# Optimization experiments

Hardware: AMD Instinct MI355X
Metric: run time of the kernel (lower is better)

The kernel has to match this reference:

```python
import jax, jax.numpy as jnp
import numpy as np

DIM = 192; NH = 6; WS = 8; SS = 4
D_INNER = 384; D_STATE = 64; MNH = 6; HEADDIM = 64; DCONV = 4; CHUNK = 128


def layernorm(x, w, b):
    m = jnp.mean(x, axis=-1, keepdims=True)
    v = jnp.var(x, axis=-1, keepdims=True)
    return (x - m) * jax.lax.rsqrt(v + 1e-5) * w + b


def segsum(a):
    # a: (..., T) -> (..., T, T) with [i,j] = sum_{k=j+1..i} a_k (lower-tri), -inf-ish above diag
    T = a.shape[-1]
    x = jnp.broadcast_to(a[..., None], a.shape + (T,))
    lo = np.tril(np.ones((T, T), dtype=bool), -1)
    x = jnp.where(lo, x, 0.0)
    s = jnp.cumsum(x, axis=-2)
    keep = np.tril(np.ones((T, T), dtype=bool), 0)
    return jnp.where(keep, s, -1e9)


def ssd(X, a, Bm, Cm):
    # Mamba2 chunked state-space dual scan. X:(b,l,h,p) a:(b,l,h) Bm/Cm:(b,l,n)
    b, l, h, p = X.shape
    n = Bm.shape[-1]
    nc = l // CHUNK
    Xc = X.reshape(b, nc, CHUNK, h, p)
    ac = a.reshape(b, nc, CHUNK, h).transpose(0, 3, 1, 2)  # (b,h,c,cl)
    Bc = Bm.reshape(b, nc, CHUNK, n)
    Cc = Cm.reshape(b, nc, CHUNK, n)
    a_cs = jnp.cumsum(ac, axis=-1)
    Lm = jnp.exp(segsum(ac))  # (b,h,c,cl,cl)
    Y_diag = jnp.einsum('bcln,bcsn,bhcls,bcshp->bclhp', Cc, Bc, Lm, Xc)
    decay_states = jnp.exp(a_cs[..., -1:] - a_cs)
    states = jnp.einsum('bcln,bhcl,bclhp->bchpn', Bc, decay_states, Xc)
    a_last = jnp.pad(a_cs[..., -1], ((0, 0), (0, 0), (1, 0)))
    decay_chunk = jnp.exp(segsum(a_last))  # (b,h,c+1,c+1)
    states_cat = jnp.concatenate([jnp.zeros_like(states[:, :1]), states], axis=1)
    prev = jnp.einsum('bhzc,bchpn->bzhpn', decay_chunk, states_cat)[:, :-1]
    Y_off = jnp.einsum('bcln,bchpn,bhcl->bclhp', Cc, prev, jnp.exp(a_cs))
    return (Y_diag + Y_off).reshape(b, l, h, p)


def mamba2(xs, in_w, conv_w, conv_b, dt_bias, A_log, D, norm_w, out_w):
    b, l, _ = xs.shape
    zxbcdt = xs @ in_w.T  # (b,l,2*di+2*n+nh)
    z = zxbcdt[..., :D_INNER]
    xBC = zxbcdt[..., D_INNER:2 * D_INNER + 2 * D_STATE]
    dt = jax.nn.softplus(zxbcdt[..., -MNH:] + dt_bias)
    # causal depthwise conv1d
    xt = xBC.transpose(0, 2, 1)
    xt = jax.lax.conv_general_dilated(xt, conv_w[:, None, :], (1,), [(DCONV - 1, 0)],
                                      feature_group_count=xt.shape[1],
                                      dimension_numbers=('NCH', 'OIH', 'NCH'))
    xBC = jax.nn.silu((xt + conv_b[None, :, None]).transpose(0, 2, 1))
    xp = xBC[..., :D_INNER].reshape(b, l, MNH, HEADDIM)
    Bm = xBC[..., D_INNER:D_INNER + D_STATE]
    Cm = xBC[..., D_INNER + D_STATE:]
    A = -jnp.exp(A_log)
    y = ssd(xp * dt[..., None], dt * A, Bm, Cm)
    y = y + xp * D[None, None, :, None]
    y = y.reshape(b, l, D_INNER)
    y = y * jax.nn.silu(z)  # gated RMSNorm
    y = y * jax.lax.rsqrt(jnp.mean(y * y, axis=-1, keepdims=True) + 1e-5) * norm_w
    return y @ out_w.T


def build_mask(H, W):
    img = np.zeros((H, W))
    cnt = 0
    for hs in (slice(0, -WS), slice(-WS, -SS), slice(-SS, None)):
        for wsl in (slice(0, -WS), slice(-WS, -SS), slice(-SS, None)):
            img[hs, wsl] = cnt
            cnt += 1
    mw = img.reshape(H // WS, WS, W // WS, WS).transpose(0, 2, 1, 3).reshape(-1, WS * WS)
    diff = mw[:, None, :] - mw[:, :, None]
    return jnp.asarray(np.where(diff != 0, -100.0, 0.0).astype(np.float32))


def gated_window_attn(xw, mask, qkv_w, qkv_b, proj_w, proj_b, gate_w, gate_b):
    Bw, N, C = xw.shape
    hd = C // NH
    qkv = (xw @ qkv_w.T + qkv_b).reshape(Bw, N, 3, NH, hd).transpose(2, 0, 3, 1, 4)
    q, k, v = qkv[0], qkv[1], qkv[2]
    s = jnp.einsum('bhnd,bhmd->bhnm', q, k) * (hd ** -0.5)
    nW = mask.shape[0]
    s = (s.reshape(Bw // nW, nW, NH, N, N) + mask[None, :, None]).reshape(Bw, NH, N, N)
    a = jax.nn.softmax(s, axis=-1)
    o = jnp.einsum('bhnm,bhmd->bhnd', a, v).transpose(0, 2, 1, 3)  # (Bw,N,NH,hd)
    gate = jax.nn.sigmoid(xw @ gate_w.T + gate_b)  # per-head gate from pre-attn x
    o = (o * gate[..., None]).reshape(Bw, N, C)
    return o @ proj_w.T + proj_b


def lgs_forward(x, H, W, n1_w, n1_b, m_in_w, m_conv_w, m_conv_b, m_dt_bias, m_A_log,
                m_D, m_norm_w, m_out_w, qkv_w, qkv_b, proj_w, proj_b, gate_w, gate_b,
                fus_w, fus_b, eca_w, n2_w, n2_b, fc1_w, fc1_b, fc2_w, fc2_b):
    twoB, L, C = x.shape
    Bh = twoB // 2
    shortcut = x
    xn = layernorm(x, n1_w, n1_b)
    # Mamba branch: interleave frame0/frame1 tokens -> (Bh, 2L, C) scan -> de-interleave
    xs = jnp.stack([xn[:Bh], xn[Bh:]], axis=2).reshape(Bh, 2 * L, C)
    ym = mamba2(xs, m_in_w, m_conv_w, m_conv_b, m_dt_bias, m_A_log, m_D, m_norm_w, m_out_w)
    ym = ym.reshape(Bh, L, 2, C)
    x_mamba = jnp.concatenate([ym[:, :, 0], ym[:, :, 1]], axis=0)  # (2B,L,C)
    # shifted-window gated attention branch
    x2 = jnp.roll(xn.reshape(twoB, H, W, C), (-SS, -SS), axis=(1, 2))
    xw = x2.reshape(twoB, H // WS, WS, W // WS, WS, C).transpose(0, 1, 3, 2, 4, 5).reshape(-1, WS * WS, C)
    ow = gated_window_attn(xw, build_mask(H, W), qkv_w, qkv_b, proj_w, proj_b, gate_w, gate_b)
    ow = ow.reshape(twoB, H // WS, W // WS, WS, WS, C).transpose(0, 1, 3, 2, 4, 5).reshape(twoB, H, W, C)
    x_attn = jnp.roll(ow, (SS, SS), axis=(1, 2)).reshape(twoB, L, C)
    # fusion 1x1 conv == per-pixel linear over concatenated channels
    xf = jnp.concatenate([x_mamba, x_attn], axis=-1) @ fus_w.T + fus_b
    # ECAB: global-avg-pool channel attention via k=3 1D conv over channels
    pooled = jnp.pad(jnp.mean(xf, axis=1), ((0, 0), (1, 1)))
    ca = jax.nn.sigmoid(eca_w[0] * pooled[:, :-2] + eca_w[1] * pooled[:, 1:-1] + eca_w[2] * pooled[:, 2:])
    xf = xf * ca[:, None, :]
    xo = shortcut + xf
    h = layernorm(xo, n2_w, n2_b)
    h = jax.nn.gelu(h @ fc1_w.T + fc1_b, approximate=False) @ fc2_w.T + fc2_b
    return xo + h


def setup_inputs() -> dict:
    key = jax.random.key(0)
    ks = jax.random.split(key, 12)
    C = DIM

    def w(k, shape, s=0.02):
        return jax.random.normal(k, shape, jnp.float32) * s

    return {
        'x': jax.random.normal(ks[0], (4, 2304, C), jnp.float32),
        'H': 48, 'W': 48,
        'n1_w': jnp.ones((C,), jnp.float32), 'n1_b': jnp.zeros((C,), jnp.float32),
        'm_in_w': w(ks[1], (2 * D_INNER + 2 * D_STATE + MNH, C)),
        'm_conv_w': w(ks[2], (D_INNER + 2 * D_STATE, DCONV), 0.1),
        'm_conv_b': jnp.zeros((D_INNER + 2 * D_STATE,), jnp.float32),
        'm_dt_bias': jnp.log(jnp.expm1(jnp.full((MNH,), 0.01, jnp.float32))),
        'm_A_log': jnp.log(jnp.arange(1, MNH + 1, dtype=jnp.float32)),
        'm_D': jnp.ones((MNH,), jnp.float32),
        'm_norm_w': jnp.ones((D_INNER,), jnp.float32),
        'm_out_w': w(ks[3], (C, D_INNER)),
        'qkv_w': w(ks[4], (3 * C, C)), 'qkv_b': jnp.zeros((3 * C,), jnp.float32),
        'proj_w': w(ks[5], (C, C)), 'proj_b': jnp.zeros((C,), jnp.float32),
        'gate_w': w(ks[6], (NH, C)), 'gate_b': jnp.zeros((NH,), jnp.float32),
        'fus_w': w(ks[7], (C, 2 * C)), 'fus_b': jnp.zeros((C,), jnp.float32),
        'eca_w': w(ks[8], (3,), 0.3),
        'n2_w': jnp.ones((C,), jnp.float32), 'n2_b': jnp.zeros((C,), jnp.float32),
        'fc1_w': w(ks[9], (4 * C, C)), 'fc1_b': jnp.zeros((4 * C,), jnp.float32),
        'fc2_w': w(ks[10], (C, 4 * C)), 'fc2_b': jnp.zeros((C,), jnp.float32),
    }


def reference(x, H, W, n1_w, n1_b, m_in_w, m_conv_w, m_conv_b, m_dt_bias, m_A_log,
              m_D, m_norm_w, m_out_w, qkv_w, qkv_b, proj_w, proj_b, gate_w, gate_b,
              fus_w, fus_b, eca_w, n2_w, n2_b, fc1_w, fc1_b, fc2_w, fc2_b):
    return lgs_forward(x, H, W, n1_w, n1_b, m_in_w, m_conv_w, m_conv_b, m_dt_bias,
                       m_A_log, m_D, m_norm_w, m_out_w, qkv_w, qkv_b, proj_w, proj_b,
                       gate_w, gate_b, fus_w, fus_b, eca_w, n2_w, n2_b,
                       fc1_w, fc1_b, fc2_w, fc2_b)
```

## Files before the change

kernel.cpp:

```cpp
#include <hip/hip_runtime.h>
#include <math.h>

#define DEV __device__ __forceinline__

typedef __attribute__((ext_vector_type(8))) short short8;
typedef __attribute__((ext_vector_type(4))) float f32x4;

DEV float sigmoidf_(float x){ return 1.f/(1.f+__expf(-x)); }
DEV float siluf_(float x){ return x/(1.f+__expf(-x)); }
DEV float softplusf_(float x){ return (x>20.f)? x : log1pf(__expf(x)); }

DEV short bf16rne(float f){
  unsigned u=__float_as_uint(f);
  unsigned r=(u + 0x7FFFu + ((u>>16)&1u))>>16;
  return (short)r;
}
DEV unsigned short bf16u(float f){ return (unsigned short)bf16rne(f); }
DEV float b2f(unsigned short u){ return __uint_as_float(((unsigned)u)<<16); }
DEV float b2fs(short u){ return __uint_as_float(((unsigned)(unsigned short)u)<<16); }

DEV void gll16(const void* g, void* l){
  __builtin_amdgcn_global_load_lds(
      (const __attribute__((address_space(1))) void*)g,
      (__attribute__((address_space(3))) void*)(unsigned)(uintptr_t)l,
      16, 0, 0);
}

DEV int map_row(int r, int mode){
  if(mode==1){
    int b=r/4608; int gl=r-b*4608;
    return ((gl&1)*2+b)*2304 + (gl>>1);
  }
  if(mode==2){
    int widx=r>>6, n=r&63;
    int b=widx/36, t=widx-b*36;
    int wi=t/6, wj=t-wi*6;
    int h2=wi*8+(n>>3), w2=wj*8+(n&7);
    int ho=h2+4; if(ho>=48) ho-=48;
    int wo=w2+4; if(wo>=48) wo-=48;
    return b*2304 + ho*48 + wo;
  }
  return r;
}

__global__ __launch_bounds__(256) void k_w2b(const float* __restrict__ w0,const float* __restrict__ w1,
    const float* __restrict__ w2,const float* __restrict__ w3,const float* __restrict__ w4,
    const float* __restrict__ w5,const float* __restrict__ w6, short* __restrict__ dst){
  int seg=blockIdx.y;
  int i=blockIdx.x*256+threadIdx.x;
  const float* src; int size, off;
  switch(seg){
    case 0: src=w0; size=173184; off=0;      break;
    case 1: src=w1; size=110592; off=173184; break;
    case 2: src=w2; size=73728;  off=283776; break;
    case 3: src=w3; size=36864;  off=357504; break;
    case 4: src=w4; size=73728;  off=394368; break;
    case 5: src=w5; size=147456; off=468096; break;
    default:src=w6; size=147456; off=615552; break;
  }
  if(i<size) dst[off+i]=bf16rne(src[i]);
}

__global__ __launch_bounds__(256) void k_ln(const float* __restrict__ in, const float* __restrict__ w,
                                            const float* __restrict__ b, short* __restrict__ out){
  int warp=threadIdx.x>>6, lane=threadIdx.x&63;
  int row=blockIdx.x*4+warp;
  const float* ip=in+(size_t)row*192;
  float v0=ip[lane], v1=ip[lane+64], v2=ip[lane+128];
  float s=v0+v1+v2, sq=v0*v0+v1*v1+v2*v2;
  #pragma unroll
  for(int off=32;off;off>>=1){ s+=__shfl_xor(s,off); sq+=__shfl_xor(sq,off); }
  float mean=s*(1.f/192.f), var=sq*(1.f/192.f)-mean*mean;
  float inv=rsqrtf(var+1e-5f);
  short* op=out+(size_t)row*192;
  op[lane]    =bf16rne((v0-mean)*inv*w[lane]    +b[lane]);
  op[lane+64] =bf16rne((v1-mean)*inv*w[lane+64] +b[lane+64]);
  op[lane+128]=bf16rne((v2-mean)*inv*w[lane+128]+b[lane+128]);
}

template<int K>
__global__ __launch_bounds__(256,4) void k_gemm(const short* __restrict__ A, const short* __restrict__ W,
    const float* __restrict__ bias, const float* __restrict__ res,
    float* __restrict__ Of, short* __restrict__ Ob,
    int N, int ldo, int col_off, int gmode, int smode, int epi){
  constexpr int NP=K/64;
  __shared__ short sMem[16384];
  short (*sA)[64][64]=(short(*)[64][64])sMem;
  short (*sB)[64][64]=(short(*)[64][64])(sMem+8192);
  float* sO=(float*)sMem;
  int tid=threadIdx.x, lane=tid&63, wid=tid>>6;
  int m16=lane&15, kq=lane>>4;
  int bm=blockIdx.x*64, bn=blockIdx.y*64;
  int lrow=lane>>3;
  int lcol=((lane&7)^lrow)<<3;
  int sx=(m16&7)<<3;
  const short* ap[2]; const short* wp[2];
  #pragma unroll
  for(int t=0;t<2;t++){
    int i8=wid+t*4;
    int arow=map_row(bm+i8*8+lrow,gmode);
    ap[t]=A+(size_t)arow*K+lcol;
    int n=bn+i8*8+lrow;
    if(n>=N) n=N-1;
    wp[t]=W+(size_t)n*K+lcol;
  }
  f32x4 acc[4];
  #pragma unroll
  for(int ni=0;ni<4;ni++) acc[ni]=(f32x4){0.f,0.f,0.f,0.f};

  auto stage=[&](int p,int b){
    #pragma unroll
    for(int t=0;t<2;t++){
      int i8=wid+t*4;
      gll16(ap[t]+p*64, &sA[b][i8*8][0]);
      gll16(wp[t]+p*64, &sB[b][i8*8][0]);
    }
  };
  auto compute=[&](int p,int b){
    __builtin_amdgcn_s_setprio(1);
    #pragma unroll
    for(int half=0;half<2;half++){
      int k2=(half*32 + kq*8) ^ sx;
      short8 af=*(const short8*)&sA[b][wid*16+m16][k2];
      #pragma unroll
      for(int ni=0;ni<4;ni++){
        short8 bf=*(const short8*)&sB[b][ni*16+m16][k2];
        acc[ni]=__builtin_amdgcn_mfma_f32_16x16x32_bf16(af,bf,acc[ni],0,0,0);
      }
    }
    __builtin_amdgcn_s_setprio(0);
  };

  stage(0,0);
  if(NP>1) stage(1,1);
  #pragma unroll
  for(int p=0;p<NP;p++){
    if(p+1<NP) asm volatile("s_waitcnt vmcnt(4)":::"memory");
    else       asm volatile("s_waitcnt vmcnt(0)":::"memory");
    __builtin_amdgcn_s_barrier();
    compute(p,p&1);
    if(p+2<NP){
      __builtin_amdgcn_s_barrier();
      stage(p+2,p&1);
    }
  }

  __syncthreads();
  {
    int mbase=wid*16+4*kq;
    #pragma unroll
    for(int ni=0;ni<4;ni++)
      #pragma unroll
      for(int r=0;r<4;r++)
        sO[(mbase+r)*65 + ni*16+m16]=acc[ni][r];
  }
  __syncthreads();
  int erow=tid>>3, c0=(tid&7)*8;
  #pragma unroll
  for(int rd=0;rd<2;rd++){
    int ml=rd*32+erow;
    int m=bm+ml;
    int orow=map_row(m,smode);
    float v[8];
    #pragma unroll
    for(int j=0;j<8;j++) v[j]=sO[ml*65+c0+j];
    const float* rp=res? res+(size_t)orow*ldo+col_off : nullptr;
    #pragma unroll
    for(int j=0;j<8;j++){
      int nn=bn+c0+j;
      float val=v[j];
      if(bias && nn<N) val+=bias[nn];
      if(epi==2) val=0.5f*val*(1.f+erff(val*0.70710678118654752f));
      else if(epi==3) val+=rp[nn];
      v[j]=val;
    }
    size_t obase=(size_t)orow*ldo+col_off+bn+c0;
    if(bn+c0+7<N){
      if(Ob){
        short8 w;
        #pragma unroll
        for(int j=0;j<8;j++) w[j]=bf16rne(v[j]);
        *(short8*)(Ob+obase)=w;
      } else {
        float4 f0={v[0],v[1],v[2],v[3]}, f1={v[4],v[5],v[6],v[7]};
        *(float4*)(Of+obase)=f0;
        *(float4*)(Of+obase+4)=f1;
      }
    } else {
      #pragma unroll
      for(int j=0;j<8;j++){
        int nn=bn+c0+j;
        if(nn<N){ if(Ob) Ob[obase+j]=bf16rne(v[j]); else Of[obase+j]=v[j]; }
      }
    }
  }
}

__global__ __launch_bounds__(256) void k_conv(const short* __restrict__ zx, const float* __restrict__ cw,
                       const float* __restrict__ cb, short* __restrict__ xbc){
  int idx=blockIdx.x*256+threadIdx.x;
  if(idx>=2*4608*64) return;
  int ch0=(idx&63)*8; int rl=idx>>6;
  int l=rl%4608;
  const short* base=zx+(size_t)rl*904+384+ch0;
  short8 x0=*(const short8*)(base);
  short8 x1={0,0,0,0,0,0,0,0},x2=x1,x3=x1;
  if(l>=1) x1=*(const short8*)(base-904);
  if(l>=2) x2=*(const short8*)(base-2*904);
  if(l>=3) x3=*(const short8*)(base-3*904);
  short8 out;
  #pragma unroll
  for(int j=0;j<8;j++){
    float4 w=*(const float4*)(cw+(ch0+j)*4);
    float acc=cb[ch0+j]
      + b2fs(x3[j])*w.x + b2fs(x2[j])*w.y + b2fs(x1[j])*w.z + b2fs(x0[j])*w.w;
    out[j]=bf16rne(siluf_(acc));
  }
  *(short8*)(xbc+(size_t)rl*512+ch0)=out;
}

__global__ __launch_bounds__(128) void k_prep(const short* __restrict__ zx, const float* __restrict__ dt_bias,
    const float* __restrict__ A_log, float* __restrict__ dtb, float* __restrict__ acs, float* __restrict__ csum){
  int bid=blockIdx.x;
  int c=bid%36, h=(bid/36)%6, b=bid/216;
  int l=threadIdx.x;
  int row=b*4608+c*128+l;
  float xv=b2fs(zx[(size_t)row*904+896+h])+dt_bias[h];
  float dt=softplusf_(xv);
  float a=-__expf(A_log[h])*dt;
  dtb[row*6+h]=dt;
  __shared__ float sb[128];
  sb[l]=a; __syncthreads();
  for(int off=1;off<128;off<<=1){
    float add=(l>=off)? sb[l-off]:0.f;
    __syncthreads();
    sb[l]+=add;
    __syncthreads();
  }
  acs[((size_t)(b*6+h)*36+c)*128+l]=sb[l];
  if(l==127) csum[(b*6+h)*36+c]=sb[127];
}

__global__ __launch_bounds__(256) void k_ssd_a(const short* __restrict__ xbc, const float* __restrict__ dtb,
    const float* __restrict__ acs, const float* __restrict__ csum,
    short* __restrict__ st, float* __restrict__ Y){
  int bid=blockIdx.x;
  int h=bid%6, c=(bid/6)%36, b=bid/216;
  __shared__ unsigned short sB[128][68];
  __shared__ unsigned short sC[128][68];
  __shared__ unsigned short sXdT[64][132];
  __shared__ unsigned short sBTE[64][132];
  __shared__ unsigned short sM[128][36];
  __shared__ float sAcs[128];
  __shared__ float sE[128];
  int tid=threadIdx.x;
  int lane=tid&63, wid=tid>>6;
  int m16=lane&15, kq=lane>>4;
  int base_row=b*4608+c*128;
  const float* acsp=acs+((size_t)(b*6+h)*36+c)*128;
  float tot=csum[(b*6+h)*36+c];
  if(tid<128){ float a=acsp[tid]; sAcs[tid]=a; sE[tid]=__expf(tot-a); }
  __syncthreads();
  for(int i=tid;i<1024;i+=256){
    int l=i>>3, n0=(i&7)*8;
    int row=base_row+l;
    const short* rp=xbc+(size_t)row*512;
    short8 Bv=*(const short8*)(rp+384+n0);
    short8 Cv=*(const short8*)(rp+448+n0);
    short8 Xv=*(const short8*)(rp+h*64+n0);
    float dt=dtb[row*6+h];
    float e=sE[l];
    *(short8*)&sB[l][n0]=Bv;
    *(short8*)&sC[l][n0]=Cv;
    #pragma unroll
    for(int j=0;j<8;j++){
      sXdT[n0+j][l]=bf16u(b2fs(Xv[j])*dt);
      sBTE[n0+j][l]=bf16u(b2fs(Bv[j])*e);
    }
  }
  __syncthreads();
  {
    int wr=wid>>1, wc=wid&1;
    f32x4 accS[2][2];
    #pragma unroll
    for(int mi=0;mi<2;mi++)
      #pragma unroll
      for(int ni=0;ni<2;ni++) accS[mi][ni]=(f32x4){0.f,0.f,0.f,0.f};
    #pragma unroll
    for(int ks=0;ks<4;ks++){
      short8 a0=*(const short8*)&sXdT[wr*32+m16][ks*32+kq*8];
      short8 a1=*(const short8*)&sXdT[wr*32+16+m16][ks*32+kq*8];
      short8 b0=*(const short8*)&sBTE[wc*32+m16][ks*32+kq*8];
      short8 b1=*(const short8*)&sBTE[wc*32+16+m16][ks*32+kq*8];
      accS[0][0]=__builtin_amdgcn_mfma_f32_16x16x32_bf16(a0,b0,accS[0][0],0,0,0);
      accS[0][1]=__builtin_amdgcn_mfma_f32_16x16x32_bf16(a0,b1,accS[0][1],0,0,0);
      accS[1][0]=__builtin_amdgcn_mfma_f32_16x16x32_bf16(a1,b0,accS[1][0],0,0,0);
      accS[1][1]=__builtin_amdgcn_mfma_f32_16x16x32_bf16(a1,b1,accS[1][1],0,0,0);
    }
    short* op=st+((size_t)((b*36+c)*6+h))*4096;
    #pragma unroll
    for(int mi=0;mi<2;mi++)
      #pragma unroll
      for(int ni=0;ni<2;ni++)
        #pragma unroll
        for(int r=0;r<4;r++){
          int p=wr*32+mi*16+4*kq+r, n=wc*32+ni*16+m16;
          op[p*64+n]=bf16rne(accS[mi][ni][r]);
        }
  }
  #pragma unroll
  for(int ti=0;ti<2;ti++){
    int t = ti? (7-wid) : wid;
    f32x4 accY[4];
    #pragma unroll
    for(int pi=0;pi<4;pi++) accY[pi]=(f32x4){0.f,0.f,0.f,0.f};
    int nslab=(t>>1)+1;
    for(int jt=0;jt<nslab;jt++){
      f32x4 accD[2];
      accD[0]=(f32x4){0.f,0.f,0.f,0.f}; accD[1]=(f32x4){0.f,0.f,0.f,0.f};
      #pragma unroll
      for(int ks=0;ks<2;ks++){
        short8 a =*(const short8*)&sC[t*16+m16][ks*32+kq*8];
        short8 b0=*(const short8*)&sB[jt*32+m16][ks*32+kq*8];
        short8 b1=*(const short8*)&sB[jt*32+16+m16][ks*32+kq*8];
        accD[0]=__builtin_amdgcn_mfma_f32_16x16x32_bf16(a,b0,accD[0],0,0,0);
        accD[1]=__builtin_amdgcn_mfma_f32_16x16x32_bf16(a,b1,accD[1],0,0,0);
      }
      int lrow=t*16+4*kq;
      #pragma unroll
      for(int sti=0;sti<2;sti++)
        #pragma unroll
        for(int r=0;r<4;r++){
          int l=lrow+r, s=jt*32+sti*16+m16;
          float v=(s<=l)? __expf(sAcs[l]-sAcs[s])*accD[sti][r] : 0.f;
          sM[l][sti*16+m16]=bf16u(v);
        }
      short8 am=*(const short8*)&sM[t*16+m16][kq*8];
      #pragma unroll
      for(int pi=0;pi<4;pi++){
        short8 bx=*(const short8*)&sXdT[pi*16+m16][jt*32+kq*8];
        accY[pi]=__builtin_amdgcn_mfma_f32_16x16x32_bf16(am,bx,accY[pi],0,0,0);
      }
    }
    #pragma unroll
    for(int pi=0;pi<4;pi++)
      #pragma unroll
      for(int r=0;r<4;r++){
        int l=t*16+4*kq+r, p=pi*16+m16;
        Y[(size_t)(base_row+l)*384+h*64+p]=accY[pi][r];
      }
  }
}

__global__ __launch_bounds__(256) void k_scan(const short* __restrict__ st, const float* __restrict__ csum,
                                              short* __restrict__ prevb){
  int bid=blockIdx.x;
  int seg=bid&15, bh=bid>>4;
  int b=bh/6, h=bh%6;
  __shared__ float sE[36];
  if(threadIdx.x<36) sE[threadIdx.x]=__expf(csum[(b*6+h)*36+threadIdx.x]);
  __syncthreads();
  int e=seg*256+threadIdx.x;
  size_t stride=(size_t)6*4096;
  size_t idx=((size_t)((b*36+0)*6+h))*4096+e;
  float carry=0.f;
  for(int c4=0;c4<36;c4+=4){
    float v[4];
    #pragma unroll
    for(int j=0;j<4;j++) v[j]=b2fs(st[idx+j*stride]);
    #pragma unroll
    for(int j=0;j<4;j++){
      prevb[idx+j*stride]=bf16rne(carry);
      carry=carry*sE[c4+j]+v[j];
    }
    idx+=4*stride;
  }
}

__global__ __launch_bounds__(256) void k_ssd_b(const short* __restrict__ xbc, const short* __restrict__ prevb,
    const float* __restrict__ acs, const float* __restrict__ Dv, float* __restrict__ Y){
  int bid=blockIdx.x;
  int h=bid%6, c=(bid/6)%36, b=bid/216;
  __shared__ unsigned short sC[128][68];
  __shared__ unsigned short sP[64][68];
  __shared__ float sAcs[128];
  int tid=threadIdx.x;
  int lane=tid&63, wid=tid>>6;
  int m16=lane&15, kq=lane>>4;
  int base_row=b*4608+c*128;
  const float* acsp=acs+((size_t)(b*6+h)*36+c)*128;
  if(tid<128) sAcs[tid]=acsp[tid];
  for(int i=tid;i<1024;i+=256){
    int l=i>>3, n0=(i&7)*8;
    short8 Cv=*(const short8*)(xbc+(size_t)(base_row+l)*512+448+n0);
    *(short8*)&sC[l][n0]=Cv;
  }
  const short* pp=prevb+((size_t)((b*36+c)*6+h))*4096;
  for(int i=tid;i<512;i+=256){
    int p_=i>>3, n0=(i&7)*8;
    short8 Pv=*(const short8*)(pp+p_*64+n0);
    *(short8*)&sP[p_][n0]=Pv;
  }
  __syncthreads();
  float Dh=Dv[h];
  int lt0=2*wid;
  f32x4 acc[2][4];
  #pragma unroll
  for(int li=0;li<2;li++)
    #pragma unroll
    for(int pi=0;pi<4;pi++) acc[li][pi]=(f32x4){0.f,0.f,0.f,0.f};
  #pragma unroll
  for(int ks=0;ks<2;ks++){
    short8 a0=*(const short8*)&sC[lt0*16+m16][ks*32+kq*8];
    short8 a1=*(const short8*)&sC[(lt0+1)*16+m16][ks*32+kq*8];
    #pragma unroll
    for(int pi=0;pi<4;pi++){
      short8 bp=*(const short8*)&sP[pi*16+m16][ks*32+kq*8];
      acc[0][pi]=__builtin_amdgcn_mfma_f32_16x16x32_bf16(a0,bp,acc[0][pi],0,0,0);
      acc[1][pi]=__builtin_amdgcn_mfma_f32_16x16x32_bf16(a1,bp,acc[1][pi],0,0,0);
    }
  }
  #pragma unroll
  for(int li=0;li<2;li++){
    #pragma unroll
    for(int r=0;r<4;r++){
      int l=(lt0+li)*16+4*kq+r;
      int row=base_row+l;
      float e=__expf(sAcs[l]);
      #pragma unroll
      for(int pi=0;pi<4;pi++){
        int p=pi*16+m16;
        size_t yi=(size_t)row*384+h*64+p;
        float xpv=b2fs(xbc[(size_t)row*512+h*64+p]);
        Y[yi]+=acc[li][pi][r]*e+xpv*Dh;
      }
    }
  }
}

__global__ __launch_bounds__(256) void k_rmsgate(const float* __restrict__ Y, const short* __restrict__ zx,
    const float* __restrict__ nw, short* __restrict__ yn){
  int warp=threadIdx.x>>6, lane=threadIdx.x&63;
  int row=blockIdx.x*4+warp;
  float v[6]; float ss=0.f;
  #pragma unroll
  for(int j=0;j<6;j++){
    int cidx=lane+64*j;
    float y=Y[(size_t)row*384+cidx];
    float z=b2fs(zx[(size_t)row*904+cidx]);
    y*=siluf_(z);
    v[j]=y; ss+=y*y;
  }
  #pragma unroll
  for(int off=32;off;off>>=1) ss+=__shfl_xor(ss,off);
  float sc=rsqrtf(ss*(1.f/384.f)+1e-5f);
  #pragma unroll
  for(int j=0;j<6;j++){
    int cidx=lane+64*j;
    yn[(size_t)row*384+cidx]=bf16rne(v[j]*sc*nw[cidx]);
  }
}

__global__ __launch_bounds__(128) void k_att2(const short* __restrict__ qkv, const short* __restrict__ xn,
    const float* __restrict__ gw, const float* __restrict__ gb, short* __restrict__ obuf){
  int bid=blockIdx.x;
  int widx=bid/6, head=bid-widx*6;
  int b=widx/36, t=widx-b*36;
  int wi=t/6, wj=t-wi*6;
  int n=threadIdx.x&63, half=threadIdx.x>>6;
  __shared__ float sK[64][32], sV[64][32];
  __shared__ float sO2[64][32];
  __shared__ float sM2[64], sD2[64];
  const short* qp=qkv+(size_t)(widx*64+n)*576+head*32;
  float q[32];
  {
    short8 v0=*(const short8*)(qp),    v1=*(const short8*)(qp+8);
    short8 v2=*(const short8*)(qp+16), v3=*(const short8*)(qp+24);
    #pragma unroll
    for(int i=0;i<8;i++){ q[i]=b2fs(v0[i]); q[8+i]=b2fs(v1[i]); q[16+i]=b2fs(v2[i]); q[24+i]=b2fs(v3[i]); }
    short8 k0=*(const short8*)(qp+192+half*16), k1=*(const short8*)(qp+200+half*16);
    short8 u0=*(const short8*)(qp+384+half*16), u1=*(const short8*)(qp+392+half*16);
    #pragma unroll
    for(int i=0;i<8;i++){
      sK[n][half*16+i]=b2fs(k0[i]); sK[n][half*16+8+i]=b2fs(k1[i]);
      sV[n][half*16+i]=b2fs(u0[i]); sV[n][half*16+8+i]=b2fs(u1[i]);
    }
  }
  int h2=wi*8+(n>>3), w2=wj*8+(n&7);
  int rh=(h2<40)?0:((h2<44)?1:2);
  int rw=(w2<40)?0:((w2<44)?1:2);
  int myid=rh*3+rw;
  __syncthreads();
  const float scale=0.17677669529663687f;
  float p[32]; float mx=-1e30f;
  #pragma unroll 4
  for(int jj=0;jj<32;jj++){
    int j=half*32+jj;
    float sc=0;
    #pragma unroll
    for(int d=0;d<32;d++) sc+=q[d]*sK[j][d];
    int hj=wi*8+(j>>3), wjj=wj*8+(j&7);
    int rhj=(hj<40)?0:((hj<44)?1:2);
    int rwj=(wjj<40)?0:((wjj<44)?1:2);
    float m=((rhj*3+rwj)!=myid)? -100.f:0.f;
    float v=sc*scale+m;
    p[jj]=v; mx=fmaxf(mx,v);
  }
  float den=0;
  #pragma unroll
  for(int jj=0;jj<32;jj++){ p[jj]=__expf(p[jj]-mx); den+=p[jj]; }
  float o[32];
  #pragma unroll
  for(int d=0;d<32;d++) o[d]=0.f;
  #pragma unroll 4
  for(int jj=0;jj<32;jj++){
    float pj=p[jj];
    #pragma unroll
    for(int d=0;d<32;d++) o[d]+=pj*sV[half*32+jj][d];
  }
  if(half==1){
    sM2[n]=mx; sD2[n]=den;
    #pragma unroll
    for(int d=0;d<32;d++) sO2[n][d]=o[d];
  }
  __syncthreads();
  if(half==0){
    float m1=sM2[n], d1=sD2[n];
    float m=fmaxf(mx,m1);
    float e0=__expf(mx-m), e1=__expf(m1-m);
    float dent=den*e0+d1*e1;
    int xrow=map_row(widx*64+n,2);
    const short* xp=xn+(size_t)xrow*192;
    const float* gwp=gw+head*192;
    float g=0;
    #pragma unroll
    for(int c=0;c<24;c++){
      short8 xv=*(const short8*)(xp+c*8);
      float4 w0=*(const float4*)(gwp+c*8);
      float4 w1=*(const float4*)(gwp+c*8+4);
      g+=b2fs(xv[0])*w0.x+b2fs(xv[1])*w0.y+b2fs(xv[2])*w0.z+b2fs(xv[3])*w0.w
        +b2fs(xv[4])*w1.x+b2fs(xv[5])*w1.y+b2fs(xv[6])*w1.z+b2fs(xv[7])*w1.w;
    }
    g=sigmoidf_(g+gb[head]);
    float fac=g/dent;
    short* op=obuf+(size_t)(widx*64+n)*192+head*32;
    #pragma unroll
    for(int v8=0;v8<4;v8++){
      short8 w;
      #pragma unroll
      for(int j=0;j<8;j++){
        int d=v8*8+j;
        w[j]=bf16rne((o[d]*e0+sO2[n][d]*e1)*fac);
      }
      *(short8*)(op+v8*8)=w;
    }
  }
}

__global__ __launch_bounds__(192) void k_pool1(const float* __restrict__ xf, float* __restrict__ partial){
  int bid=blockIdx.x; int b=bid/18, seg=bid%18;
  int cidx=threadIdx.x;
  const float* p=xf+((size_t)b*2304+seg*128)*192+cidx;
  float s=0;
  for(int l=0;l<128;l++) s+=p[(size_t)l*192];
  partial[bid*192+cidx]=s;
}

__global__ __launch_bounds__(768) void k_ca(const float* __restrict__ partial, const float* __restrict__ ecaw,
                                            float* __restrict__ ca){
  int tid=threadIdx.x;
  int b=tid/192, cidx=tid%192;
  float s=0;
  for(int k=0;k<18;k++) s+=partial[(b*18+k)*192+cidx];
  float pv=s*(1.f/2304.f);
  __shared__ float sP[768];
  sP[tid]=pv; __syncthreads();
  float left =(cidx>0)?   sP[tid-1]:0.f;
  float right=(cidx<191)? sP[tid+1]:0.f;
  ca[tid]=sigmoidf_(ecaw[0]*left+ecaw[1]*pv+ecaw[2]*right);
}

__global__ __launch_bounds__(256) void k_xoln(const float* __restrict__ x, const float* __restrict__ xf,
    const float* __restrict__ ca, const float* __restrict__ w, const float* __restrict__ bvec,
    float* __restrict__ xo, short* __restrict__ out){
  int warp=threadIdx.x>>6, lane=threadIdx.x&63;
  int row=blockIdx.x*4+warp;
  int bidx=row/2304;
  const float* cap=ca+bidx*192;
  const float* xp=x+(size_t)row*192;
  const float* fp=xf+(size_t)row*192;
  float v0=xp[lane]    +fp[lane]    *cap[lane];
  float v1=xp[lane+64] +fp[lane+64] *cap[lane+64];
  float v2=xp[lane+128]+fp[lane+128]*cap[lane+128];
  float* op=xo+(size_t)row*192;
  op[lane]=v0; op[lane+64]=v1; op[lane+128]=v2;
  float s=v0+v1+v2, sq=v0*v0+v1*v1+v2*v2;
  #pragma unroll
  for(int off=32;off;off>>=1){ s+=__shfl_xor(s,off); sq+=__shfl_xor(sq,off); }
  float mean=s*(1.f/192.f), var=sq*(1.f/192.f)-mean*mean;
  float inv=rsqrtf(var+1e-5f);
  short* bp=out+(size_t)row*192;
  bp[lane]    =bf16rne((v0-mean)*inv*w[lane]    +bvec[lane]);
  bp[lane+64] =bf16rne((v1-mean)*inv*w[lane+64] +bvec[lane+64]);
  bp[lane+128]=bf16rne((v2-mean)*inv*w[lane+128]+bvec[lane+128]);
}

extern "C" void kernel_launch(void* const* d_in, const int* in_sizes, int n_in,
                              void* d_out, int out_size, void* d_ws, size_t ws_size,
                              hipStream_t stream){
  const float* x     =(const float*)d_in[0];
  const float* n1w   =(const float*)d_in[3];
  const float* n1b   =(const float*)d_in[4];
  const float* m_in_w=(const float*)d_in[5];
  const float* m_cw  =(const float*)d_in[6];
  const float* m_cb  =(const float*)d_in[7];
  const float* m_dtb =(const float*)d_in[8];
  const float* m_Al  =(const float*)d_in[9];
  const float* m_D   =(const float*)d_in[10];
  const float* m_nw  =(const float*)d_in[11];
  const float* m_ow  =(const float*)d_in[12];
  const float* qkvw  =(const float*)d_in[13];
  const float* qkvb  =(const float*)d_in[14];
  const float* projw =(const float*)d_in[15];
  const float* projb =(const float*)d_in[16];
  const float* gatew =(const float*)d_in[17];
  const float* gateb =(const float*)d_in[18];
  const float* fusw  =(const float*)d_in[19];
  const float* fusb  =(const float*)d_in[20];
  const float* ecaw  =(const float*)d_in[21];
  const float* n2w   =(const float*)d_in[22];
  const float* n2b   =(const float*)d_in[23];
  const float* fc1w  =(const float*)d_in[24];
  const float* fc1b  =(const float*)d_in[25];
  const float* fc2w  =(const float*)d_in[26];
  const float* fc2b  =(const float*)d_in[27];
  float* out=(float*)d_out;
  float* ws=(float*)d_ws;

  short* xn_bf  = (short*)(ws + 0);
  short* wb     = (short*)(ws + 884736);
  short* zx_bf  = (short*)(ws + 1266240);
  short* xbc_bf = (short*)(ws + 5431872);
  float* dtb    = ws + 7791168;
  float* acs    = ws + 7846464;
  float* csum   = ws + 7901760;
  short* st_bf  = (short*)(ws + 7902272);
  short* prevb_bf=(short*)(ws + 9671744);
  float* Y      = ws + 11441216;
  float* bigbf  = ws + 14980160;
  short* hbuf_bf= xn_bf;
  short* obuf_bf= xbc_bf;
  short* xcat_bf= prevb_bf;
  float* xf     = (float*)st_bf;
  float* xo     = Y;
  short* yn_bf  = (short*)bigbf;
  short* qkv_bf = (short*)bigbf;
  short* h1_bf  = (short*)bigbf;
  float* partial= dtb;
  float* ca     = acs;
  short* wb_in  = wb + 0;
  short* wb_qkv = wb + 173184;
  short* wb_out = wb + 283776;
  short* wb_proj= wb + 357504;
  short* wb_fus = wb + 394368;
  short* wb_fc1 = wb + 468096;
  short* wb_fc2 = wb + 615552;

  k_w2b<<<dim3(677,7),256,0,stream>>>(m_in_w,qkvw,m_ow,projw,fusw,fc1w,fc2w,wb);
  k_ln<<<2304,256,0,stream>>>(x,n1w,n1b,xn_bf);
  k_gemm<192><<<dim3(144,15),256,0,stream>>>(xn_bf,wb_in,nullptr,nullptr,nullptr,zx_bf, 902,904,0, 1,0,0);
  k_conv<<<2304,256,0,stream>>>(zx_bf,m_cw,m_cb,xbc_bf);
  k_prep<<<432,128,0,stream>>>(zx_bf,m_dtb,m_Al,dtb,acs,csum);
  k_ssd_a<<<432,256,0,stream>>>(xbc_bf,dtb,acs,csum,st_bf,Y);
  k_scan<<<192,256,0,stream>>>(st_bf,csum,prevb_bf);
  k_ssd_b<<<432,256,0,stream>>>(xbc_bf,prevb_bf,acs,m_D,Y);
  k_rmsgate<<<2304,256,0,stream>>>(Y,zx_bf,m_nw,yn_bf);
  k_gemm<384><<<dim3(144,3),256,0,stream>>>(yn_bf,wb_out,nullptr,nullptr,nullptr,xcat_bf, 192,384,0, 0,1,0);
  k_gemm<192><<<dim3(144,9),256,0,stream>>>(xn_bf,wb_qkv,qkvb,nullptr,nullptr,qkv_bf, 576,576,0, 2,0,0);
  k_att2<<<864,128,0,stream>>>(qkv_bf,xn_bf,gatew,gateb,obuf_bf);
  k_gemm<192><<<dim3(144,3),256,0,stream>>>(obuf_bf,wb_proj,projb,nullptr,nullptr,xcat_bf, 192,384,192, 0,2,0);
  k_gemm<384><<<dim3(144,3),256,0,stream>>>(xcat_bf,wb_fus,fusb,nullptr,xf,nullptr, 192,192,0, 0,0,0);
  k_pool1<<<72,192,0,stream>>>(xf,partial);
  k_ca<<<1,768,0,stream>>>(partial,ecaw,ca);
  k_xoln<<<2304,256,0,stream>>>(x,xf,ca,n2w,n2b,xo,hbuf_bf);
  k_gemm<192><<<dim3(144,12),256,0,stream>>>(hbuf_bf,wb_fc1,fc1b,nullptr,nullptr,h1_bf, 768,768,0, 0,0,2);
  k_gemm<768><<<dim3(144,3),256,0,stream>>>(h1_bf,wb_fc2,fc2b,xo,out,nullptr, 192,192,0, 0,0,3);
}
```

Baseline: 175.1 us.

## Fuse small kernels, store Y in bf16, fold pooling into fusion GEMM

```diff
diff --git a/kernel.cpp b/kernel.cpp
--- a/kernel.cpp
+++ b/kernel.cpp
@@ -43,46 +43,12 @@
   return r;
 }
 
-__global__ __launch_bounds__(256) void k_w2b(const float* __restrict__ w0,const float* __restrict__ w1,
-    const float* __restrict__ w2,const float* __restrict__ w3,const float* __restrict__ w4,
-    const float* __restrict__ w5,const float* __restrict__ w6, short* __restrict__ dst){
-  int seg=blockIdx.y;
-  int i=blockIdx.x*256+threadIdx.x;
-  const float* src; int size, off;
-  switch(seg){
-    case 0: src=w0; size=173184; off=0;      break;
-    case 1: src=w1; size=110592; off=173184; break;
-    case 2: src=w2; size=73728;  off=283776; break;
-    case 3: src=w3; size=36864;  off=357504; break;
-    case 4: src=w4; size=73728;  off=394368; break;
-    case 5: src=w5; size=147456; off=468096; break;
-    default:src=w6; size=147456; off=615552; break;
-  }
-  if(i<size) dst[off+i]=bf16rne(src[i]);
-}
-
-__global__ __launch_bounds__(256) void k_ln(const float* __restrict__ in, const float* __restrict__ w,
-                                            const float* __restrict__ b, short* __restrict__ out){
-  int warp=threadIdx.x>>6, lane=threadIdx.x&63;
-  int row=blockIdx.x*4+warp;
-  const float* ip=in+(size_t)row*192;
-  float v0=ip[lane], v1=ip[lane+64], v2=ip[lane+128];
-  float s=v0+v1+v2, sq=v0*v0+v1*v1+v2*v2;
-  #pragma unroll
-  for(int off=32;off;off>>=1){ s+=__shfl_xor(s,off); sq+=__shfl_xor(sq,off); }
-  float mean=s*(1.f/192.f), var=sq*(1.f/192.f)-mean*mean;
-  float inv=rsqrtf(var+1e-5f);
-  short* op=out+(size_t)row*192;
-  op[lane]    =bf16rne((v0-mean)*inv*w[lane]    +b[lane]);
-  op[lane+64] =bf16rne((v1-mean)*inv*w[lane+64] +b[lane+64]);
-  op[lane+128]=bf16rne((v2-mean)*inv*w[lane+128]+b[lane+128]);
-}
-
 template<int K>
-__global__ __launch_bounds__(256,4) void k_gemm(const short* __restrict__ A, const short* __restrict__ W,
+DEV void gemm_body(const short* __restrict__ A, const short* __restrict__ W,
     const float* __restrict__ bias, const float* __restrict__ res,
     float* __restrict__ Of, short* __restrict__ Ob,
-    int N, int ldo, int col_off, int gmode, int smode, int epi){
+    int N, int ldo, int col_off, int gmode, int smode, int epi,
+    int bx, int by, float* __restrict__ pool){
   constexpr int NP=K/64;
   __shared__ short sMem[16384];
   short (*sA)[64][64]=(short(*)[64][64])sMem;
@@ -90,7 +56,7 @@
   float* sO=(float*)sMem;
   int tid=threadIdx.x, lane=tid&63, wid=tid>>6;
   int m16=lane&15, kq=lane>>4;
-  int bm=blockIdx.x*64, bn=blockIdx.y*64;
+  int bm=bx*64, bn=by*64;
   int lrow=lane>>3;
   int lcol=((lane&7)^lrow)<<3;
   int sx=(m16&7)<<3;
@@ -194,56 +160,127 @@
       }
     }
   }
-}
-
-__global__ __launch_bounds__(256) void k_conv(const short* __restrict__ zx, const float* __restrict__ cw,
-                       const float* __restrict__ cb, short* __restrict__ xbc){
-  int idx=blockIdx.x*256+threadIdx.x;
-  if(idx>=2*4608*64) return;
-  int ch0=(idx&63)*8; int rl=idx>>6;
-  int l=rl%4608;
-  const short* base=zx+(size_t)rl*904+384+ch0;
-  short8 x0=*(const short8*)(base);
-  short8 x1={0,0,0,0,0,0,0,0},x2=x1,x3=x1;
-  if(l>=1) x1=*(const short8*)(base-904);
-  if(l>=2) x2=*(const short8*)(base-2*904);
-  if(l>=3) x3=*(const short8*)(base-3*904);
-  short8 out;
-  #pragma unroll
-  for(int j=0;j<8;j++){
-    float4 w=*(const float4*)(cw+(ch0+j)*4);
-    float acc=cb[ch0+j]
-      + b2fs(x3[j])*w.x + b2fs(x2[j])*w.y + b2fs(x1[j])*w.z + b2fs(x0[j])*w.w;
-    out[j]=bf16rne(siluf_(acc));
-  }
-  *(short8*)(xbc+(size_t)rl*512+ch0)=out;
-}
-
-__global__ __launch_bounds__(128) void k_prep(const short* __restrict__ zx, const float* __restrict__ dt_bias,
-    const float* __restrict__ A_log, float* __restrict__ dtb, float* __restrict__ acs, float* __restrict__ csum){
+  if(pool){
+    if(tid<64){
+      float s=0;
+      #pragma unroll 8
+      for(int ml=0;ml<64;ml++) s+=sO[ml*65+tid];
+      if(bias) s+=64.f*bias[bn+tid];
+      atomicAdd(&pool[(bm/2304)*192 + bn+tid], s);
+    }
+  }
+}
+
+template<int K>
+__global__ __launch_bounds__(256,4) void k_gemm(const short* __restrict__ A, const short* __restrict__ W,
+    const float* __restrict__ bias, const float* __restrict__ res,
+    float* __restrict__ Of, short* __restrict__ Ob,
+    int N, int ldo, int col_off, int gmode, int smode, int epi, float* __restrict__ pool){
+  gemm_body<K>(A,W,bias,res,Of,Ob,N,ldo,col_off,gmode,smode,epi,blockIdx.x,blockIdx.y,pool);
+}
+
+__global__ __launch_bounds__(256,4) void k_gemm_inqkv(const short* __restrict__ xn,
+    const short* __restrict__ w_in, short* __restrict__ zx,
+    const short* __restrict__ w_qkv, const float* __restrict__ qkvb, short* __restrict__ qkv){
+  if(blockIdx.y<15)
+    gemm_body<192>(xn,w_in,nullptr,nullptr,nullptr,zx, 902,904,0, 1,0,0, blockIdx.x,blockIdx.y, nullptr);
+  else
+    gemm_body<192>(xn,w_qkv,qkvb,nullptr,nullptr,qkv, 576,576,0, 2,0,0, blockIdx.x,blockIdx.y-15, nullptr);
+}
+
+__global__ __launch_bounds__(256) void k_lnw2b(const float* __restrict__ in, const float* __restrict__ w,
+    const float* __restrict__ b, short* __restrict__ out,
+    const float* __restrict__ w0,const float* __restrict__ w1,const float* __restrict__ w2,
+    const float* __restrict__ w3,const float* __restrict__ w4,const float* __restrict__ w5,
+    const float* __restrict__ w6, short* __restrict__ dst){
   int bid=blockIdx.x;
-  int c=bid%36, h=(bid/36)%6, b=bid/216;
-  int l=threadIdx.x;
-  int row=b*4608+c*128+l;
-  float xv=b2fs(zx[(size_t)row*904+896+h])+dt_bias[h];
-  float dt=softplusf_(xv);
-  float a=-__expf(A_log[h])*dt;
-  dtb[row*6+h]=dt;
-  __shared__ float sb[128];
-  sb[l]=a; __syncthreads();
-  for(int off=1;off<128;off<<=1){
-    float add=(l>=off)? sb[l-off]:0.f;
+  if(bid<2304){
+    int warp=threadIdx.x>>6, lane=threadIdx.x&63;
+    int row=bid*4+warp;
+    const float* ip=in+(size_t)row*192;
+    float v0=ip[lane], v1=ip[lane+64], v2=ip[lane+128];
+    float s=v0+v1+v2, sq=v0*v0+v1*v1+v2*v2;
+    #pragma unroll
+    for(int off=32;off;off>>=1){ s+=__shfl_xor(s,off); sq+=__shfl_xor(sq,off); }
+    float mean=s*(1.f/192.f), var=sq*(1.f/192.f)-mean*mean;
+    float inv=rsqrtf(var+1e-5f);
+    short* op=out+(size_t)row*192;
+    op[lane]    =bf16rne((v0-mean)*inv*w[lane]    +b[lane]);
+    op[lane+64] =bf16rne((v1-mean)*inv*w[lane+64] +b[lane+64]);
+    op[lane+128]=bf16rne((v2-mean)*inv*w[lane+128]+b[lane+128]);
+  } else {
+    int flat=bid-2304;
+    int seg=flat/677;
+    int i=(flat-seg*677)*256+threadIdx.x;
+    const float* src; int size, off;
+    switch(seg){
+      case 0: src=w0; size=173184; off=0;      break;
+      case 1: src=w1; size=110592; off=173184; break;
+      case 2: src=w2; size=73728;  off=283776; break;
+      case 3: src=w3; size=36864;  off=357504; break;
+      case 4: src=w4; size=73728;  off=394368; break;
+      case 5: src=w5; size=147456; off=468096; break;
+      default:src=w6; size=147456; off=615552; break;
+    }
+    if(i<size) dst[off+i]=bf16rne(src[i]);
+  }
+}
+
+__global__ __launch_bounds__(256) void k_convprep(const short* __restrict__ zx, const float* __restrict__ cw,
+    const float* __restrict__ cb, short* __restrict__ xbc,
+    const float* __restrict__ dt_bias, const float* __restrict__ A_log,
+    float* __restrict__ dtb, float* __restrict__ acs, float* __restrict__ csum){
+  int bid=blockIdx.x;
+  if(bid<2304){
+    int idx=bid*256+threadIdx.x;
+    int ch0=(idx&63)*8; int rl=idx>>6;
+    int l=rl%4608;
+    const short* base=zx+(size_t)rl*904+384+ch0;
+    short8 x0=*(const short8*)(base);
+    short8 x1={0,0,0,0,0,0,0,0},x2=x1,x3=x1;
+    if(l>=1) x1=*(const short8*)(base-904);
+    if(l>=2) x2=*(const short8*)(base-2*904);
+    if(l>=3) x3=*(const short8*)(base-3*904);
+    short8 out;
+    #pragma unroll
+    for(int j=0;j<8;j++){
+      float4 w=*(const float4*)(cw+(ch0+j)*4);
+      float acc=cb[ch0+j]
+        + b2fs(x3[j])*w.x + b2fs(x2[j])*w.y + b2fs(x1[j])*w.z + b2fs(x0[j])*w.w;
+      out[j]=bf16rne(siluf_(acc));
+    }
+    *(short8*)(xbc+(size_t)rl*512+ch0)=out;
+  } else {
+    int pb=bid-2304;
+    int c=pb%36, h=(pb/36)%6, b=pb/216;
+    int l=threadIdx.x;
+    __shared__ float sb[128];
+    float a=0.f;
+    if(l<128){
+      int row=b*4608+c*128+l;
+      float xv=b2fs(zx[(size_t)row*904+896+h])+dt_bias[h];
+      float dt=softplusf_(xv);
+      a=-__expf(A_log[h])*dt;
+      dtb[row*6+h]=dt;
+      sb[l]=a;
+    }
     __syncthreads();
-    sb[l]+=add;
-    __syncthreads();
-  }
-  acs[((size_t)(b*6+h)*36+c)*128+l]=sb[l];
-  if(l==127) csum[(b*6+h)*36+c]=sb[127];
+    for(int off=1;off<128;off<<=1){
+      float add=(l>=off && l<128)? sb[l-off]:0.f;
+      __syncthreads();
+      if(l<128) sb[l]+=add;
+      __syncthreads();
+    }
+    if(l<128){
+      acs[((size_t)(b*6+h)*36+c)*128+l]=sb[l];
+      if(l==127) csum[(b*6+h)*36+c]=sb[127];
+    }
+  }
 }
 
 __global__ __launch_bounds__(256) void k_ssd_a(const short* __restrict__ xbc, const float* __restrict__ dtb,
     const float* __restrict__ acs, const float* __restrict__ csum,
-    short* __restrict__ st, float* __restrict__ Y){
+    short* __restrict__ st, short* __restrict__ Y){
   int bid=blockIdx.x;
   int h=bid%6, c=(bid/6)%36, b=bid/216;
   __shared__ unsigned short sB[128][68];
@@ -347,7 +384,7 @@
       #pragma unroll
       for(int r=0;r<4;r++){
         int l=t*16+4*kq+r, p=pi*16+m16;
-        Y[(size_t)(base_row+l)*384+h*64+p]=accY[pi][r];
+        Y[(size_t)(base_row+l)*384+h*64+p]=bf16rne(accY[pi][r]);
       }
   }
 }
@@ -378,7 +415,7 @@
 }
 
 __global__ __launch_bounds__(256) void k_ssd_b(const short* __restrict__ xbc, const short* __restrict__ prevb,
-    const float* __restrict__ acs, const float* __restrict__ Dv, float* __restrict__ Y){
+    const float* __restrict__ acs, const float* __restrict__ Dv, short* __restrict__ Y){
   int bid=blockIdx.x;
   int h=bid%6, c=(bid/6)%36, b=bid/216;
   __shared__ unsigned short sC[128][68];
@@ -432,21 +469,25 @@
         int p=pi*16+m16;
         size_t yi=(size_t)row*384+h*64+p;
         float xpv=b2fs(xbc[(size_t)row*512+h*64+p]);
-        Y[yi]+=acc[li][pi][r]*e+xpv*Dh;
+        Y[yi]=bf16rne(b2fs(Y[yi])+acc[li][pi][r]*e+xpv*Dh);
       }
     }
   }
 }
 
-__global__ __launch_bounds__(256) void k_rmsgate(const float* __restrict__ Y, const short* __restrict__ zx,
-    const float* __restrict__ nw, short* __restrict__ yn){
+__global__ __launch_bounds__(256) void k_rmsgate(const short* __restrict__ Y, const short* __restrict__ zx,
+    const float* __restrict__ nw, short* __restrict__ yn, float* __restrict__ partial){
+  if(blockIdx.x<3){
+    int t=blockIdx.x*256+threadIdx.x;
+    if(t<768) partial[t]=0.f;
+  }
   int warp=threadIdx.x>>6, lane=threadIdx.x&63;
   int row=blockIdx.x*4+warp;
   float v[6]; float ss=0.f;
   #pragma unroll
   for(int j=0;j<6;j++){
     int cidx=lane+64*j;
-    float y=Y[(size_t)row*384+cidx];
+    float y=b2fs(Y[(size_t)row*384+cidx]);
     float z=b2fs(zx[(size_t)row*904+cidx]);
     y*=siluf_(z);
     v[j]=y; ss+=y*y;
@@ -557,22 +598,11 @@
   }
 }
 
-__global__ __launch_bounds__(192) void k_pool1(const float* __restrict__ xf, float* __restrict__ partial){
-  int bid=blockIdx.x; int b=bid/18, seg=bid%18;
-  int cidx=threadIdx.x;
-  const float* p=xf+((size_t)b*2304+seg*128)*192+cidx;
-  float s=0;
-  for(int l=0;l<128;l++) s+=p[(size_t)l*192];
-  partial[bid*192+cidx]=s;
-}
-
 __global__ __launch_bounds__(768) void k_ca(const float* __restrict__ partial, const float* __restrict__ ecaw,
                                             float* __restrict__ ca){
   int tid=threadIdx.x;
-  int b=tid/192, cidx=tid%192;
-  float s=0;
-  for(int k=0;k<18;k++) s+=partial[(b*18+k)*192+cidx];
-  float pv=s*(1.f/2304.f);
+  int cidx=tid%192;
+  float pv=partial[tid]*(1.f/2304.f);
   __shared__ float sP[768];
   sP[tid]=pv; __syncthreads();
   float left =(cidx>0)?   sP[tid-1]:0.f;
@@ -646,15 +676,15 @@
   float* csum   = ws + 7901760;
   short* st_bf  = (short*)(ws + 7902272);
   short* prevb_bf=(short*)(ws + 9671744);
-  float* Y      = ws + 11441216;
+  short* Y_bf   = (short*)(ws + 11441216);
   float* bigbf  = ws + 14980160;
+  short* qkv_bf = (short*)(ws + 18519104);
   short* hbuf_bf= xn_bf;
   short* obuf_bf= xbc_bf;
   short* xcat_bf= prevb_bf;
   float* xf     = (float*)st_bf;
-  float* xo     = Y;
+  float* xo     = (float*)Y_bf;
   short* yn_bf  = (short*)bigbf;
-  short* qkv_bf = (short*)bigbf;
   short* h1_bf  = (short*)bigbf;
   float* partial= dtb;
   float* ca     = acs;
@@ -666,23 +696,19 @@
   short* wb_fc1 = wb + 468096;
   short* wb_fc2 = wb + 615552;
 
-  k_w2b<<<dim3(677,7),256,0,stream>>>(m_in_w,qkvw,m_ow,projw,fusw,fc1w,fc2w,wb);
-  k_ln<<<2304,256,0,stream>>>(x,n1w,n1b,xn_bf);
-  k_gemm<192><<<dim3(144,15),256,0,stream>>>(xn_bf,wb_in,nullptr,nullptr,nullptr,zx_bf, 902,904,0, 1,0,0);
-  k_conv<<<2304,256,0,stream>>>(zx_bf,m_cw,m_cb,xbc_bf);
-  k_prep<<<432,128,0,stream>>>(zx_bf,m_dtb,m_Al,dtb,acs,csum);
-  k_ssd_a<<<432,256,0,stream>>>(xbc_bf,dtb,acs,csum,st_bf,Y);
+  k_lnw2b<<<7043,256,0,stream>>>(x,n1w,n1b,xn_bf, m_in_w,qkvw,m_ow,projw,fusw,fc1w,fc2w,wb);
+  k_gemm_inqkv<<<dim3(144,24),256,0,stream>>>(xn_bf,wb_in,zx_bf,wb_qkv,qkvb,qkv_bf);
+  k_convprep<<<2736,256,0,stream>>>(zx_bf,m_cw,m_cb,xbc_bf, m_dtb,m_Al,dtb,acs,csum);
+  k_ssd_a<<<432,256,0,stream>>>(xbc_bf,dtb,acs,csum,st_bf,Y_bf);
   k_scan<<<192,256,0,stream>>>(st_bf,csum,prevb_bf);
-  k_ssd_b<<<432,256,0,stream>>>(xbc_bf,prevb_bf,acs,m_D,Y);
-  k_rmsgate<<<2304,256,0,stream>>>(Y,zx_bf,m_nw,yn_bf);
-  k_gemm<384><<<dim3(144,3),256,0,stream>>>(yn_bf,wb_out,nullptr,nullptr,nullptr,xcat_bf, 192,384,0, 0,1,0);
-  k_gemm<192><<<dim3(144,9),256,0,stream>>>(xn_bf,wb_qkv,qkvb,nullptr,nullptr,qkv_bf, 576,576,0, 2,0,0);
+  k_ssd_b<<<432,256,0,stream>>>(xbc_bf,prevb_bf,acs,m_D,Y_bf);
+  k_rmsgate<<<2304,256,0,stream>>>(Y_bf,zx_bf,m_nw,yn_bf,partial);
+  k_gemm<384><<<dim3(144,3),256,0,stream>>>(yn_bf,wb_out,nullptr,nullptr,nullptr,xcat_bf, 192,384,0, 0,1,0, nullptr);
   k_att2<<<864,128,0,stream>>>(qkv_bf,xn_bf,gatew,gateb,obuf_bf);
-  k_gemm<192><<<dim3(144,3),256,0,stream>>>(obuf_bf,wb_proj,projb,nullptr,nullptr,xcat_bf, 192,384,192, 0,2,0);
-  k_gemm<384><<<dim3(144,3),256,0,stream>>>(xcat_bf,wb_fus,fusb,nullptr,xf,nullptr, 192,192,0, 0,0,0);
-  k_pool1<<<72,192,0,stream>>>(xf,partial);
+  k_gemm<192><<<dim3(144,3),256,0,stream>>>(obuf_bf,wb_proj,projb,nullptr,nullptr,xcat_bf, 192,384,192, 0,2,0, nullptr);
+  k_gemm<384><<<dim3(144,3),256,0,stream>>>(xcat_bf,wb_fus,fusb,nullptr,xf,nullptr, 192,192,0, 0,0,0, partial);
   k_ca<<<1,768,0,stream>>>(partial,ecaw,ca);
   k_xoln<<<2304,256,0,stream>>>(x,xf,ca,n2w,n2b,xo,hbuf_bf);
-  k_gemm<192><<<dim3(144,12),256,0,stream>>>(hbuf_bf,wb_fc1,fc1b,nullptr,nullptr,h1_bf, 768,768,0, 0,0,2);
-  k_gemm<768><<<dim3(144,3),256,0,stream>>>(h1_bf,wb_fc2,fc2b,xo,out,nullptr, 192,192,0, 0,0,3);
-}
+  k_gemm<192><<<dim3(144,12),256,0,stream>>>(hbuf_bf,wb_fc1,fc1b,nullptr,nullptr,h1_bf, 768,768,0, 0,0,2, nullptr);
+  k_gemm<768><<<dim3(144,3),256,0,stream>>>(h1_bf,wb_fc2,fc2b,xo,out,nullptr, 192,192,0, 0,0,3, nullptr);
+}
```

Result: faster. 170.7 us (-2.6%).
